# Optimization experiments

Hardware: AMD Instinct MI355X
Metric: run time of the kernel (lower is better)

## Reference

```python
import jax, jax.numpy as jnp
import numpy as np

B = 1024
NUM_DENSE = 13
NUM_SPARSE = 26
VOCAB = 100000
EMB_DIM = 16
BOT = [512, 256, 64, 16]
TOP = [1024, 512, 256]
D_INT = BOT[-1] + NUM_SPARSE * EMB_DIM  # 432
OUT_INT = D_INT * (D_INT + 1) // 2      # 93528


def setup_inputs() -> dict:
    key = jax.random.key(0)
    ks = jax.random.split(key, 32)
    inp = {
        "dense_features": jax.random.normal(ks[0], (B, NUM_DENSE), jnp.float32),
        "sparse_features": jax.random.randint(ks[1], (B, NUM_SPARSE), 0, VOCAB),
        "emb_tables": jax.random.normal(ks[2], (NUM_SPARSE, VOCAB, EMB_DIM), jnp.float32) * 0.02,
    }
    # bottom MLP weights (in, out) convention
    dims = [NUM_DENSE] + BOT
    for i in range(len(BOT)):
        inp[f"bw{i}"] = jax.random.normal(ks[3 + i], (dims[i], dims[i + 1]), jnp.float32) * 0.02
        inp[f"bb{i}"] = jnp.zeros((dims[i + 1],), jnp.float32)
    tdims = [BOT[-1] + OUT_INT] + TOP + [1]
    for i in range(len(TOP) + 1):
        inp[f"tw{i}"] = jax.random.normal(ks[10 + i], (tdims[i], tdims[i + 1]), jnp.float32) * 0.02
        inp[f"tb{i}"] = jnp.zeros((tdims[i + 1],), jnp.float32)
    return inp


def _forward(dense_features, emb_tables, bws, bbs, tws, tbs, sparse_features):
    # bottom MLP: Linear+ReLU stacks
    h = dense_features
    for w, b in zip(bws, bbs):
        h = jax.nn.relu(h @ w + b)
    dense_out = h  # (B, 16)
    # embedding lookups: table t indexed by column t of sparse_features
    # emb_tables: (F, V, E); gather per-table then flatten -> (B, F*E)
    emb = jnp.take_along_axis(
        emb_tables[None],  # (1, F, V, E)
        sparse_features.T[None, :, :, None].transpose(0, 1, 2, 3) * 0 + sparse_features.T[None, :, :, None],
        axis=2,
    )  # placeholder avoided below
    # cleaner: vmap over tables
    emb = jax.vmap(lambda tbl, idx: tbl[idx], in_axes=(0, 1))(emb_tables, sparse_features)  # (F, B, E)
    emb = jnp.transpose(emb, (1, 0, 2)).reshape(dense_features.shape[0], -1)  # (B, F*E)
    x = jnp.concatenate([dense_out, emb], axis=1)  # (B, D_INT)
    # pairwise interaction: upper triangle (incl. diagonal) of outer product.
    iu0, iu1 = np.triu_indices(x.shape[1])
    inter = x[:, iu0] * x[:, iu1]  # (B, OUT_INT) -- only needed entries
    z = jnp.concatenate([dense_out, inter], axis=1)
    n_top = len(tws)
    for i, (w, b) in enumerate(zip(tws, tbs)):
        z = z @ w + b
        if i < n_top - 1:
            z = jax.nn.relu(z)
    return z


def reference(dense_features, sparse_features, emb_tables,
              bw0, bb0, bw1, bb1, bw2, bb2, bw3, bb3,
              tw0, tb0, tw1, tb1, tw2, tb2, tw3, tb3):
    bws = [bw0, bw1, bw2, bw3]
    bbs = [bb0, bb1, bb2, bb3]
    tws = [tw0, tw1, tw2, tw3]
    tbs = [tb0, tb1, tb2, tb3]
    return _forward(dense_features, emb_tables, bws, bbs, tws, tbs, sparse_features)
```

## Files before the change

### kernel.cpp

```cpp
#include <hip/hip_runtime.h>
#include <stdint.h>

typedef unsigned short ushort_t;
typedef __attribute__((ext_vector_type(4))) float f32x4;
typedef __attribute__((ext_vector_type(8))) short s16x8;

#define DEVFN static __device__ __forceinline__

constexpr int B_   = 1024;
constexpr int P_   = 93528;
constexpr int K1   = 93544;
constexpr int Kp   = 94208;
constexpr int SPLITS = 16;
constexpr int KCH  = Kp / SPLITS;
constexpr int KSTEPS = KCH / 64;

DEVFN ushort_t f2bf(float f) {
  union { float f; unsigned int u; } x; x.f = f;
  unsigned int r = x.u + 0x7FFFu + ((x.u >> 16) & 1u);
  return (ushort_t)(r >> 16);
}

DEVFN void gload_lds16(const void* g, void* l) {
  __builtin_amdgcn_global_load_lds((const __attribute__((address_space(1))) unsigned int*)g,
                                   (__attribute__((address_space(3))) unsigned int*)l, 16, 0, 0);
}

__global__ __launch_bounds__(256) void k_pre(const float* __restrict__ dense,
    const int* __restrict__ sparse, const float* __restrict__ tbl,
    const float* __restrict__ bw0, const float* __restrict__ bb0,
    const float* __restrict__ bw1, const float* __restrict__ bb1,
    const float* __restrict__ bw2, const float* __restrict__ bb2,
    const float* __restrict__ bw3, const float* __restrict__ bb3,
    int* __restrict__ iu, float* __restrict__ xT) {
  __shared__ float sm[13520];
  int bid = blockIdx.x, t = threadIdx.x;
  if (bid < 368) {
    int k = bid * 256 + t;
    if (bid < 8) {
      int idx = bid * 256 + t;
      xT[432 * 1024 + idx] = (idx < 1024) ? 1.f : 0.f;
    }
    if (k >= Kp) return;
    int v;
    if (k < 16) v = k | (432 << 16);
    else if (k >= K1) v = 433 | (433 << 16);
    else {
      int p = k - 16;
      float s = sqrtf((float)(748225 - 8 * p));
      int i = (int)((865.0f - s) * 0.5f);
      if (i < 0) i = 0; if (i > 431) i = 431;
      while (i < 431 && (i + 1) * (865 - (i + 1)) / 2 <= p) ++i;
      while (i > 0 && i * (865 - i) / 2 > p) --i;
      int j = i + (p - i * (865 - i) / 2);
      v = i | (j << 16);
    }
    iu[k] = v;
  } else if (bid < 432) {
    float* xs = sm;
    float* h1 = sm + 208;
    float* h2 = h1 + 8192;
    float* h3 = h2 + 4096;
    int m0 = (bid - 368) * 16;
    if (t < 208) xs[t] = dense[m0 * 13 + t];
    __syncthreads();
    #pragma unroll
    for (int h = 0; h < 2; ++h) {
      int n = h * 256 + t;
      float a[16];
      float bv = bb0[n];
      #pragma unroll
      for (int r = 0; r < 16; ++r) a[r] = bv;
      for (int k = 0; k < 13; ++k) {
        float w = bw0[k * 512 + n];
        #pragma unroll
        for (int r = 0; r < 16; ++r) a[r] = fmaf(xs[r * 13 + k], w, a[r]);
      }
      #pragma unroll
      for (int r = 0; r < 16; ++r) h1[r * 512 + n] = fmaxf(a[r], 0.f);
    }
    __syncthreads();
    {
      int n = t;
      float a[16];
      float bv = bb1[n];
      #pragma unroll
      for (int r = 0; r < 16; ++r) a[r] = bv;
      for (int k = 0; k < 512; ++k) {
        float w = bw1[k * 256 + n];
        #pragma unroll
        for (int r = 0; r < 16; ++r) a[r] = fmaf(h1[r * 512 + k], w, a[r]);
      }
      #pragma unroll
      for (int r = 0; r < 16; ++r) h2[r * 256 + n] = fmaxf(a[r], 0.f);
    }
    __syncthreads();
    {
      int n = t & 63, r0 = t >> 6;
      float a[4];
      float bv = bb2[n];
      #pragma unroll
      for (int i = 0; i < 4; ++i) a[i] = bv;
      for (int k = 0; k < 256; ++k) {
        float w = bw2[k * 64 + n];
        #pragma unroll
        for (int i = 0; i < 4; ++i) a[i] = fmaf(h2[(r0 + 4 * i) * 256 + k], w, a[i]);
      }
      #pragma unroll
      for (int i = 0; i < 4; ++i) h3[(r0 + 4 * i) * 64 + n] = fmaxf(a[i], 0.f);
    }
    __syncthreads();
    {
      int n = t & 15, r = t >> 4;
      float a = bb3[n];
      for (int k = 0; k < 64; ++k) a = fmaf(h3[r * 64 + k], bw3[k * 16 + n], a);
      xT[(size_t)n * B_ + m0 + r] = fmaxf(a, 0.f);
    }
  } else {
    int e = bid - 432;
    int f = e >> 2;
    int b = (e & 3) * 256 + t;
    int idx = sparse[(size_t)b * 26 + f];
    const float4* src = (const float4*)(tbl + ((size_t)f * 100000 + idx) * 16);
    #pragma unroll
    for (int q = 0; q < 4; ++q) {
      float4 v = src[q];
      int r = 16 + f * 16 + q * 4;
      xT[(size_t)(r + 0) * B_ + b] = v.x;
      xT[(size_t)(r + 1) * B_ + b] = v.y;
      xT[(size_t)(r + 2) * B_ + b] = v.z;
      xT[(size_t)(r + 3) * B_ + b] = v.w;
    }
  }
}

__global__ __launch_bounds__(256, 4) void k_gz(const float* __restrict__ xT,
                                               const int* __restrict__ iu,
                                               const float* __restrict__ tw0,
                                               ushort_t* __restrict__ Z,
                                               ushort_t* __restrict__ WT) {
  __shared__ char smem[256 * 68 * 2];
  int bid = blockIdx.x, t = threadIdx.x;
  int r3 = bid % 3;
  if (r3 == 0) {
    int idx = bid / 3;
    int* ls_iu = (int*)smem;
    int l = t & 63, w = t >> 6;
    int mb = (idx & 15) * 64;
    int kt = (idx >> 4) * 512;
    ls_iu[t] = iu[kt + t];
    ls_iu[256 + t] = iu[kt + 256 + t];
    __syncthreads();
    uint32_t moff = mb + l;
    int kw = w * 128;
    #pragma unroll 2
    for (int g = 0; g < 16; ++g) {
      int kloc = kw + g * 8;
      int4 ij0 = *(const int4*)&ls_iu[kloc];
      int4 ij1 = *(const int4*)&ls_iu[kloc + 4];
      float p[8];
      {
        int v0 = ij0.x, v1 = ij0.y, v2 = ij0.z, v3 = ij0.w;
        p[0] = xT[(uint32_t)((v0 & 0xFFFF) << 10) + moff] * xT[(uint32_t)((v0 >> 16) << 10) + moff];
        p[1] = xT[(uint32_t)((v1 & 0xFFFF) << 10) + moff] * xT[(uint32_t)((v1 >> 16) << 10) + moff];
        p[2] = xT[(uint32_t)((v2 & 0xFFFF) << 10) + moff] * xT[(uint32_t)((v2 >> 16) << 10) + moff];
        p[3] = xT[(uint32_t)((v3 & 0xFFFF) << 10) + moff] * xT[(uint32_t)((v3 >> 16) << 10) + moff];
        v0 = ij1.x; v1 = ij1.y; v2 = ij1.z; v3 = ij1.w;
        p[4] = xT[(uint32_t)((v0 & 0xFFFF) << 10) + moff] * xT[(uint32_t)((v0 >> 16) << 10) + moff];
        p[5] = xT[(uint32_t)((v1 & 0xFFFF) << 10) + moff] * xT[(uint32_t)((v1 >> 16) << 10) + moff];
        p[6] = xT[(uint32_t)((v2 & 0xFFFF) << 10) + moff] * xT[(uint32_t)((v2 >> 16) << 10) + moff];
        p[7] = xT[(uint32_t)((v3 & 0xFFFF) << 10) + moff] * xT[(uint32_t)((v3 >> 16) << 10) + moff];
      }
      union { uint32_t w4[4]; int4 v4; } o;
      asm("v_cvt_pk_bf16_f32 %0, %1, %2" : "=v"(o.w4[0]) : "v"(p[0]), "v"(p[1]));
      asm("v_cvt_pk_bf16_f32 %0, %1, %2" : "=v"(o.w4[1]) : "v"(p[2]), "v"(p[3]));
      asm("v_cvt_pk_bf16_f32 %0, %1, %2" : "=v"(o.w4[2]) : "v"(p[4]), "v"(p[5]));
      asm("v_cvt_pk_bf16_f32 %0, %1, %2" : "=v"(o.w4[3]) : "v"(p[6]), "v"(p[7]));
      int kglob = kt + kloc;
      *(int4*)&Z[((size_t)(kglob >> 3) * 1024 + moff) * 8] = o.v4;
    }
  } else {
    int idx = (bid / 3) * 2 + r3 - 1;
    ushort_t* ls = (ushort_t*)smem;
    int k0 = (idx % 368) * 256, n0 = (idx / 368) * 64;
    int kr = t >> 2, c4 = t & 3;
    #pragma unroll
    for (int pass = 0; pass < 4; ++pass) {
      int kl = pass * 64 + kr;
      int k = k0 + kl;
      #pragma unroll
      for (int q = 0; q < 4; ++q) {
        float4 v = make_float4(0.f, 0.f, 0.f, 0.f);
        if (k < K1) v = *(const float4*)&tw0[(size_t)k * 1024 + n0 + q * 16 + c4 * 4];
        ushort_t* d = &ls[kl * 68 + q * 16 + c4 * 4];
        d[0] = f2bf(v.x); d[1] = f2bf(v.y); d[2] = f2bf(v.z); d[3] = f2bf(v.w);
      }
    }
    __syncthreads();
    int nl = t >> 2, kq = t & 3;
    ushort_t* dst = WT + (size_t)(n0 + nl) * Kp + k0 + kq * 64;
    #pragma unroll
    for (int j = 0; j < 8; ++j) {
      union { ushort_t u[8]; int4 v; } o;
      #pragma unroll
      for (int e = 0; e < 8; ++e) o.u[e] = ls[(kq * 64 + j * 8 + e) * 68 + nl];
      *(int4*)(dst + j * 8) = o.v;
    }
  }
}

__global__ __launch_bounds__(512, 2) void k_gemm(const ushort_t* __restrict__ Z,
                                                 const ushort_t* __restrict__ WT,
                                                 float* __restrict__ part) {
  __shared__ ushort_t lds[65536];
  int t = threadIdx.x;
  int bid = blockIdx.x;
  int x = bid & 7, r = bid >> 3;
  int g = (x << 3) | (r & 7);
  int s = g >> 2;
  int m0 = (g & 3) * 256, n0 = (r >> 3) * 256;
  int kb = s * KCH;

  int rr = t >> 3, cc = t & 7;
  int cs = cc ^ (rr & 7);
  const ushort_t* pa0 = Z + (((size_t)(kb >> 3) + cs) * 1024 + m0 + rr) * 8;
  const ushort_t* pb0 = WT + (size_t)(n0 + rr) * Kp + kb + cs * 8;
  const size_t rowStrideB = (size_t)64 * Kp;
  int l0 = t * 8;

  int w = t >> 6, l = t & 63;
  int wm = (w >> 2) * 128, wn = (w & 3) * 64;
  int lhi = l >> 4, llo = l & 15;

  f32x4 acc[8][4];
  #pragma unroll
  for (int a = 0; a < 8; ++a)
    #pragma unroll
    for (int b = 0; b < 4; ++b) acc[a][b] = f32x4{0.f, 0.f, 0.f, 0.f};

  #pragma unroll
  for (int i = 0; i < 4; ++i)
    gload_lds16(pb0 + i * rowStrideB, &lds[32768 + i * 4096 + l0]);
  gload_lds16(pa0,           &lds[0 * 4096 + l0]);
  gload_lds16(pa0 + 2 * 512, &lds[2 * 4096 + l0]);
  gload_lds16(pa0 + 1 * 512, &lds[1 * 4096 + l0]);
  gload_lds16(pa0 + 3 * 512, &lds[3 * 4096 + l0]);
  #pragma unroll
  for (int i = 0; i < 4; ++i)
    gload_lds16(pb0 + 64 + i * rowStrideB, &lds[32768 + 16384 + i * 4096 + l0]);

  for (int tt = 0; tt < KSTEPS; ++tt) {
    const ushort_t* Ab = &lds[(tt & 1) * 16384];
    const ushort_t* Bb = &lds[32768 + (tt & 1) * 16384];
    bool pf  = (tt + 1 < KSTEPS);
    bool pf2 = (tt + 2 < KSTEPS);
    ushort_t* dA  = &lds[((tt + 1) & 1) * 16384];
    ushort_t* dB2 = &lds[32768 + (tt & 1) * 16384];
    const ushort_t* sA  = pa0 + (size_t)(tt + 1) * 65536;
    const ushort_t* sB2 = pb0 + (size_t)(tt + 2) * 64;
    s16x8 bf[4][2];

    if (pf) asm volatile("s_waitcnt vmcnt(6)" ::: "memory");
    else    asm volatile("s_waitcnt vmcnt(2)" ::: "memory");
    asm volatile("s_waitcnt lgkmcnt(0)" ::: "memory");
    __builtin_amdgcn_s_barrier();
    if (pf) {
      gload_lds16(sA,           dA + l0);
      gload_lds16(sA + 2 * 512, dA + 2 * 4096 + l0);
    }
    #pragma unroll
    for (int nf = 0; nf < 4; ++nf)
      #pragma unroll
      for (int ks = 0; ks < 2; ++ks) {
        int row = wn + nf * 16 + llo;
        int ch = (ks * 4 + lhi) ^ (row & 7);
        bf[nf][ks] = *(const s16x8*)&Bb[row * 64 + ch * 8];
      }
    #pragma unroll
    for (int q = 0; q < 4; ++q) {
      if (q == 1 && pf) {
        gload_lds16(sA + 1 * 512, dA + 1 * 4096 + l0);
        gload_lds16(sA + 3 * 512, dA + 3 * 4096 + l0);
      }
      if (q == 2) {
        if (pf) asm volatile("s_waitcnt vmcnt(8)" ::: "memory");
        else    asm volatile("s_waitcnt vmcnt(0)" ::: "memory");
        asm volatile("s_waitcnt lgkmcnt(0)" ::: "memory");
        __builtin_amdgcn_s_barrier();
        if (pf2) {
          #pragma unroll
          for (int i = 0; i < 4; ++i)
            gload_lds16(sB2 + i * rowStrideB, dB2 + i * 4096 + l0);
        }
      }
      s16x8 af[2][2];
      #pragma unroll
      for (int j = 0; j < 2; ++j)
        #pragma unroll
        for (int ks = 0; ks < 2; ++ks) {
          int row = wm + (q * 2 + j) * 16 + llo;
          int ch = (ks * 4 + lhi) ^ (row & 7);
          af[j][ks] = *(const s16x8*)&Ab[row * 64 + ch * 8];
        }
      #pragma unroll
      for (int j = 0; j < 2; ++j)
        #pragma unroll
        for (int nf = 0; nf < 4; ++nf)
          #pragma unroll
          for (int ks = 0; ks < 2; ++ks)
            acc[q * 2 + j][nf] = __builtin_amdgcn_mfma_f32_16x16x32_bf16(af[j][ks], bf[nf][ks], acc[q * 2 + j][nf], 0, 0, 0);
    }
  }

  float* pbase = part + ((size_t)s << 20);
  #pragma unroll
  for (int mf = 0; mf < 8; ++mf)
    #pragma unroll
    for (int nf = 0; nf < 4; ++nf) {
      int n = n0 + wn + nf * 16 + llo;
      #pragma unroll
      for (int r2 = 0; r2 < 4; ++r2) {
        int m = m0 + wm + mf * 16 + lhi * 4 + r2;
        pbase[(size_t)m * 1024 + n] = acc[mf][nf][r2];
      }
    }
}

__global__ __launch_bounds__(256) void k_red(const float* __restrict__ part,
                                             const float* __restrict__ bias,
                                             float* __restrict__ z1) {
  int idx = blockIdx.x * 256 + threadIdx.x;
  float a = bias[idx & 1023];
  #pragma unroll
  for (int s = 0; s < SPLITS; ++s) a += part[((size_t)s << 20) + idx];
  z1[idx] = fmaxf(a, 0.f);
}

template<int K, int N>
__global__ __launch_bounds__(256) void k_sgemm(const float* __restrict__ A,
                                               const float* __restrict__ W,
                                               const float* __restrict__ bias,
                                               float* __restrict__ C) {
  __shared__ float As[16][34];
  __shared__ float Bs[16][68];
  int t = threadIdx.x;
  int m0 = blockIdx.x * 32, n0 = blockIdx.y * 64;
  int tx = t & 15, ty = t >> 4;
  float acc[2][4];
  #pragma unroll
  for (int j = 0; j < 2; ++j)
    #pragma unroll
    for (int q = 0; q < 4; ++q) acc[j][q] = 0.f;
  int ar = t >> 3, ak = (t & 7) * 2;
  int bk = t >> 4, bn = (t & 15) * 4;
  for (int k0 = 0; k0 < K; k0 += 16) {
    float2 av = *(const float2*)&A[(size_t)(m0 + ar) * K + k0 + ak];
    float4 bv = *(const float4*)&W[(size_t)(k0 + bk) * N + n0 + bn];
    __syncthreads();
    As[ak][ar] = av.x; As[ak + 1][ar] = av.y;
    *(float4*)&Bs[bk][bn] = bv;
    __syncthreads();
    #pragma unroll
    for (int k = 0; k < 16; ++k) {
      float2 a = *(const float2*)&As[k][ty * 2];
      float4 b = *(const float4*)&Bs[k][tx * 4];
      acc[0][0] = fmaf(a.x, b.x, acc[0][0]); acc[0][1] = fmaf(a.x, b.y, acc[0][1]);
      acc[0][2] = fmaf(a.x, b.z, acc[0][2]); acc[0][3] = fmaf(a.x, b.w, acc[0][3]);
      acc[1][0] = fmaf(a.y, b.x, acc[1][0]); acc[1][1] = fmaf(a.y, b.y, acc[1][1]);
      acc[1][2] = fmaf(a.y, b.z, acc[1][2]); acc[1][3] = fmaf(a.y, b.w, acc[1][3]);
    }
  }
  #pragma unroll
  for (int j = 0; j < 2; ++j) {
    int m = m0 + ty * 2 + j;
    float4 o;
    o.x = fmaxf(acc[j][0] + bias[n0 + tx * 4 + 0], 0.f);
    o.y = fmaxf(acc[j][1] + bias[n0 + tx * 4 + 1], 0.f);
    o.z = fmaxf(acc[j][2] + bias[n0 + tx * 4 + 2], 0.f);
    o.w = fmaxf(acc[j][3] + bias[n0 + tx * 4 + 3], 0.f);
    *(float4*)&C[(size_t)m * N + n0 + tx * 4] = o;
  }
}

__global__ __launch_bounds__(256) void k_last(const float* __restrict__ z3,
                                              const float* __restrict__ w,
                                              const float* __restrict__ bias,
                                              float* __restrict__ out) {
  int t = threadIdx.x, l = t & 63, wv = t >> 6;
  int m = blockIdx.x * 4 + wv;
  float s = 0.f;
  #pragma unroll
  for (int c = 0; c < 4; ++c) s = fmaf(z3[(size_t)m * 256 + c * 64 + l], w[c * 64 + l], s);
  #pragma unroll
  for (int off = 32; off; off >>= 1) s += __shfl_down(s, off, 64);
  if (l == 0) out[m] = s + bias[0];
}

__global__ __launch_bounds__(256) void k_z1init(const float* __restrict__ bias, float* __restrict__ z1) {
  int idx = blockIdx.x * 256 + threadIdx.x;
  z1[idx] = bias[idx & 1023];
}
__global__ __launch_bounds__(256) void k_relu(float* __restrict__ z1) {
  int idx = blockIdx.x * 256 + threadIdx.x;
  z1[idx] = fmaxf(z1[idx], 0.f);
}
constexpr int FB_S = 8;
__global__ __launch_bounds__(256) void k_fbgemm(const float* __restrict__ xT,
                                                const int* __restrict__ iu,
                                                const float* __restrict__ tw0,
                                                float* __restrict__ z1) {
  __shared__ float zs[32 * 64];
  __shared__ float wsb[32 * 64];
  int t = threadIdx.x;
  int m0 = blockIdx.x * 64, n0 = blockIdx.y * 64, s = blockIdx.z;
  int kch = (K1 + FB_S - 1) / FB_S;
  int k0 = s * kch, kend = min(k0 + kch, K1);
  float acc[16];
  #pragma unroll
  for (int q = 0; q < 16; ++q) acc[q] = 0.f;
  int mm = t & 63, ng = t >> 6;
  for (int kk = k0; kk < kend; kk += 32) {
    __syncthreads();
    for (int sl = t; sl < 2048; sl += 256) {
      int kloc = sl >> 6, v6 = sl & 63;
      int k = kk + kloc;
      float zv = 0.f, wv = 0.f;
      if (k < kend) {
        int ij = iu[k];
        int i = ij & 0xFFFF, j = ij >> 16;
        zv = xT[(size_t)i * B_ + m0 + v6] * xT[(size_t)j * B_ + m0 + v6];
        wv = tw0[(size_t)k * 1024 + n0 + v6];
      }
      zs[kloc * 64 + v6] = zv;
      wsb[kloc * 64 + v6] = wv;
    }
    __syncthreads();
    #pragma unroll 4
    for (int kloc = 0; kloc < 32; ++kloc) {
      float zv = zs[kloc * 64 + mm];
      #pragma unroll
      for (int q = 0; q < 16; ++q)
        acc[q] = fmaf(zv, wsb[kloc * 64 + ng * 16 + q], acc[q]);
    }
  }
  #pragma unroll
  for (int q = 0; q < 16; ++q)
    atomicAdd(&z1[(size_t)(m0 + mm) * 1024 + n0 + ng * 16 + q], acc[q]);
}

extern "C" void kernel_launch(void* const* d_in, const int* in_sizes, int n_in,
                              void* d_out, int out_size, void* d_ws, size_t ws_size,
                              hipStream_t stream) {
  const float* dense  = (const float*)d_in[0];
  const int*   sparse = (const int*)  d_in[1];
  const float* emb    = (const float*)d_in[2];
  const float* bw0 = (const float*)d_in[3];  const float* bb0 = (const float*)d_in[4];
  const float* bw1 = (const float*)d_in[5];  const float* bb1 = (const float*)d_in[6];
  const float* bw2 = (const float*)d_in[7];  const float* bb2 = (const float*)d_in[8];
  const float* bw3 = (const float*)d_in[9];  const float* bb3 = (const float*)d_in[10];
  const float* tw0 = (const float*)d_in[11]; const float* tb0 = (const float*)d_in[12];
  const float* tw1 = (const float*)d_in[13]; const float* tb1 = (const float*)d_in[14];
  const float* tw2 = (const float*)d_in[15]; const float* tb2 = (const float*)d_in[16];
  const float* tw3 = (const float*)d_in[17]; const float* tb3 = (const float*)d_in[18];
  float* out = (float*)d_out;

  char* ws = (char*)d_ws;
  size_t off = 0;
  auto alloc = [&](size_t bytes) -> char* {
    char* p = ws + off;
    off = (off + bytes + 255) & ~(size_t)255;
    return p;
  };
  float* xT = (float*)alloc((size_t)434 * 1024 * 4);
  int*   iu = (int*)  alloc((size_t)Kp * 4);
  float* z1 = (float*)alloc((size_t)1024 * 1024 * 4);
  float* z2 = (float*)alloc((size_t)1024 * 512 * 4);
  float* z3 = (float*)alloc((size_t)1024 * 256 * 4);
  ushort_t* Z    = (ushort_t*)alloc((size_t)1024 * Kp * 2);
  ushort_t* WT   = (ushort_t*)alloc((size_t)1024 * Kp * 2);
  float*    part = (float*)   alloc((size_t)SPLITS * 1024 * 1024 * 4);
  bool big = (off <= ws_size);

  k_pre<<<536, 256, 0, stream>>>(dense, sparse, emb, bw0, bb0, bw1, bb1, bw2, bb2, bw3, bb3, iu, xT);

  if (big) {
    k_gz<<<8832, 256, 0, stream>>>(xT, iu, tw0, Z, WT);
    k_gemm<<<256, 512, 0, stream>>>(Z, WT, part);
    k_red<<<4096, 256, 0, stream>>>(part, tb0, z1);
  } else {
    k_z1init<<<4096, 256, 0, stream>>>(tb0, z1);
    k_fbgemm<<<dim3(16, 16, FB_S), 256, 0, stream>>>(xT, iu, tw0, z1);
    k_relu<<<4096, 256, 0, stream>>>(z1);
  }

  k_sgemm<1024, 512><<<dim3(32, 8), 256, 0, stream>>>(z1, tw1, tb1, z2);
  k_sgemm<512, 256><<<dim3(32, 4), 256, 0, stream>>>(z2, tw2, tb2, z3);
  k_last<<<256, 256, 0, stream>>>(z3, tw3, tb3, out);
}
```

Baseline: 538.0 us.

## Store converted top weights in k-chunked layout matching Z, drop LDS transpose

The bf16 copy of tw0 is now written in the same [k/8][n][8] chunked layout as the interaction matrix Z, so each thread reads eight k-rows of one column and writes a 16-byte chunk directly, with no LDS transpose or barrier. The GEMM's B-operand loads switch from row-major strided addressing to contiguous chunk addressing identical to the A path. Without the shared staging buffer the conversion kernel's LDS use shrinks and launch bounds are raised to allow more resident blocks. Global reads in the conversion become per-column and coalesced across lanes, though each thread now issues more scalar loads.

```diff
diff --git a/kernel.cpp b/kernel.cpp
--- a/kernel.cpp
+++ b/kernel.cpp
@@ -134,17 +134,16 @@
   }
 }
 
-__global__ __launch_bounds__(256, 4) void k_gz(const float* __restrict__ xT,
+__global__ __launch_bounds__(256, 8) void k_gz(const float* __restrict__ xT,
                                                const int* __restrict__ iu,
                                                const float* __restrict__ tw0,
                                                ushort_t* __restrict__ Z,
                                                ushort_t* __restrict__ WT) {
-  __shared__ char smem[256 * 68 * 2];
+  __shared__ int ls_iu[512];
   int bid = blockIdx.x, t = threadIdx.x;
   int r3 = bid % 3;
   if (r3 == 0) {
     int idx = bid / 3;
-    int* ls_iu = (int*)smem;
     int l = t & 63, w = t >> 6;
     int mb = (idx & 15) * 64;
     int kt = (idx >> 4) * 512;
@@ -181,30 +180,32 @@
     }
   } else {
     int idx = (bid / 3) * 2 + r3 - 1;
-    ushort_t* ls = (ushort_t*)smem;
     int k0 = (idx % 368) * 256, n0 = (idx / 368) * 64;
-    int kr = t >> 2, c4 = t & 3;
-    #pragma unroll
-    for (int pass = 0; pass < 4; ++pass) {
-      int kl = pass * 64 + kr;
-      int k = k0 + kl;
-      #pragma unroll
-      for (int q = 0; q < 4; ++q) {
-        float4 v = make_float4(0.f, 0.f, 0.f, 0.f);
-        if (k < K1) v = *(const float4*)&tw0[(size_t)k * 1024 + n0 + q * 16 + c4 * 4];
-        ushort_t* d = &ls[kl * 68 + q * 16 + c4 * 4];
-        d[0] = f2bf(v.x); d[1] = f2bf(v.y); d[2] = f2bf(v.z); d[3] = f2bf(v.w);
-      }
-    }
-    __syncthreads();
-    int nl = t >> 2, kq = t & 3;
-    ushort_t* dst = WT + (size_t)(n0 + nl) * Kp + k0 + kq * 64;
-    #pragma unroll
-    for (int j = 0; j < 8; ++j) {
-      union { ushort_t u[8]; int4 v; } o;
-      #pragma unroll
-      for (int e = 0; e < 8; ++e) o.u[e] = ls[(kq * 64 + j * 8 + e) * 68 + nl];
-      *(int4*)(dst + j * 8) = o.v;
+    int nl = t & 63, kq = t >> 6;
+    int n = n0 + nl;
+    int kbase = k0 + kq * 64;
+    const float* src = tw0 + (size_t)kbase * 1024 + n;
+    ushort_t* dst = WT + ((size_t)(kbase >> 3) * 1024 + n) * 8;
+    bool full = (kbase + 64 <= K1);
+    #pragma unroll
+    for (int g = 0; g < 8; ++g) {
+      float v[8];
+      if (full) {
+        #pragma unroll
+        for (int e = 0; e < 8; ++e) v[e] = src[(size_t)(g * 8 + e) << 10];
+      } else {
+        #pragma unroll
+        for (int e = 0; e < 8; ++e) {
+          int k = kbase + g * 8 + e;
+          v[e] = (k < K1) ? src[(size_t)(g * 8 + e) << 10] : 0.f;
+        }
+      }
+      union { uint32_t w4[4]; int4 v4; } o;
+      asm("v_cvt_pk_bf16_f32 %0, %1, %2" : "=v"(o.w4[0]) : "v"(v[0]), "v"(v[1]));
+      asm("v_cvt_pk_bf16_f32 %0, %1, %2" : "=v"(o.w4[1]) : "v"(v[2]), "v"(v[3]));
+      asm("v_cvt_pk_bf16_f32 %0, %1, %2" : "=v"(o.w4[2]) : "v"(v[4]), "v"(v[5]));
+      asm("v_cvt_pk_bf16_f32 %0, %1, %2" : "=v"(o.w4[3]) : "v"(v[6]), "v"(v[7]));
+      *(int4*)(dst + (size_t)g * 8192) = o.v4;
     }
   }
 }
@@ -223,9 +224,8 @@
 
   int rr = t >> 3, cc = t & 7;
   int cs = cc ^ (rr & 7);
-  const ushort_t* pa0 = Z + (((size_t)(kb >> 3) + cs) * 1024 + m0 + rr) * 8;
-  const ushort_t* pb0 = WT + (size_t)(n0 + rr) * Kp + kb + cs * 8;
-  const size_t rowStrideB = (size_t)64 * Kp;
+  const ushort_t* pa0 = Z  + (((size_t)(kb >> 3) + cs) * 1024 + m0 + rr) * 8;
+  const ushort_t* pb0 = WT + (((size_t)(kb >> 3) + cs) * 1024 + n0 + rr) * 8;
   int l0 = t * 8;
 
   int w = t >> 6, l = t & 63;
@@ -240,14 +240,14 @@
 
   #pragma unroll
   for (int i = 0; i < 4; ++i)
-    gload_lds16(pb0 + i * rowStrideB, &lds[32768 + i * 4096 + l0]);
+    gload_lds16(pb0 + i * 512, &lds[32768 + i * 4096 + l0]);
   gload_lds16(pa0,           &lds[0 * 4096 + l0]);
   gload_lds16(pa0 + 2 * 512, &lds[2 * 4096 + l0]);
   gload_lds16(pa0 + 1 * 512, &lds[1 * 4096 + l0]);
   gload_lds16(pa0 + 3 * 512, &lds[3 * 4096 + l0]);
   #pragma unroll
   for (int i = 0; i < 4; ++i)
-    gload_lds16(pb0 + 64 + i * rowStrideB, &lds[32768 + 16384 + i * 4096 + l0]);
+    gload_lds16(pb0 + 65536 + i * 512, &lds[32768 + 16384 + i * 4096 + l0]);
 
   for (int tt = 0; tt < KSTEPS; ++tt) {
     const ushort_t* Ab = &lds[(tt & 1) * 16384];
@@ -257,7 +257,7 @@
     ushort_t* dA  = &lds[((tt + 1) & 1) * 16384];
     ushort_t* dB2 = &lds[32768 + (tt & 1) * 16384];
     const ushort_t* sA  = pa0 + (size_t)(tt + 1) * 65536;
-    const ushort_t* sB2 = pb0 + (size_t)(tt + 2) * 64;
+    const ushort_t* sB2 = pb0 + (size_t)(tt + 2) * 65536;
     s16x8 bf[4][2];
 
     if (pf) asm volatile("s_waitcnt vmcnt(6)" ::: "memory");
@@ -290,7 +290,7 @@
         if (pf2) {
           #pragma unroll
           for (int i = 0; i < 4; ++i)
-            gload_lds16(sB2 + i * rowStrideB, dB2 + i * 4096 + l0);
+            gload_lds16(sB2 + i * 512, dB2 + i * 4096 + l0);
         }
       }
       s16x8 af[2][2];
```

Measured after the change: 547.8 us. About the same (+1.8%).
